# Kernel optimization log

Measured on AMD Instinct MI355X. Metric: run time of the kernel, lower is better.

The kernel has to match this reference:

```python
import jax, jax.numpy as jnp
import numpy as np

B, S, D = 4, 8192, 1024

def log_g(x):
    # log of g(x): log(x + 0.5) for x >= 0, log(sigmoid(x)) = -softplus(-x) otherwise
    return jnp.where(x >= 0, jnp.log(jax.nn.relu(x) + 0.5), -jax.nn.softplus(-x))

def setup_inputs() -> dict:
    key = jax.random.key(0)
    k1, k2 = jax.random.split(key)
    x = jax.random.normal(k1, (B, S, D), dtype=jnp.float32)
    # Linear(dim, 3*dim, bias=False); stored as [dim, 3*dim] so y = x @ W
    W = jax.random.normal(k2, (D, 3 * D), dtype=jnp.float32) * (1.0 / np.sqrt(D))
    return {"x": x, "W": W}

def reference(x, W):
    # x: [B, S, D], W: [D, 3D]
    hW = jnp.einsum('bsd,de->bse', x, W)  # [B, S, 3D]
    hidden, f_gate, i_gate = jnp.split(hW, 3, axis=-1)

    # log-space normalized gates:
    # diff = softplus(-f) - softplus(-i); log_f' = -softplus(diff); log_i' = -softplus(-diff)
    diff = jax.nn.softplus(-f_gate) - jax.nn.softplus(-i_gate)
    log_f = -jax.nn.softplus(diff)
    log_i = -jax.nn.softplus(-diff)
    log_values = log_i + log_g(hidden)

    # Heinsen associative scan in log space (float32 internally)
    a_star = jnp.cumsum(log_f.astype(jnp.float32), axis=1)
    log_h0_plus_b_star = jax.lax.cumlogsumexp(log_values.astype(jnp.float32) - a_star, axis=1)
    log_h = a_star + log_h0_plus_b_star
    out = jnp.exp(log_h).astype(x.dtype)  # [B, S, D]
    return out
```

## Files before the change

kernel.cpp:

```cpp
#include <hip/hip_runtime.h>
#include <hip/hip_bf16.h>
#include <cstdint>
#include <cstddef>


#define BB 4
#define SS 8192
#define DD 1024
#define MM 32768
#define KK 1024
#define NN 3072
#define CHUNKS 256
#define CLEN 32
#define NCH 4096
#define NT 16

typedef __bf16 bf16;
typedef __bf16 bf16x2 __attribute__((ext_vector_type(2)));
typedef __bf16 bf16x4 __attribute__((ext_vector_type(4)));
typedef __bf16 bf16x8 __attribute__((ext_vector_type(8)));
typedef float f32x4 __attribute__((ext_vector_type(4)));

__device__ __forceinline__ void gload16(const bf16* g, bf16* l) {
  __builtin_amdgcn_global_load_lds(
      (const __attribute__((address_space(1))) unsigned int*)(const void*)g,
      (__attribute__((address_space(3))) unsigned int*)(void*)l,
      16, 0, 0);
}

#if __has_builtin(__builtin_amdgcn_exp2f)
#define EXP2(x) __builtin_amdgcn_exp2f(x)
#else
#define EXP2(x) __expf((x) * 0.69314718056f)
#endif

__device__ __forceinline__ void gate2(float h, float f, float i,
                                      float& F, float& IG) {
  const float NL2E = -1.44269504089f;
  float P = EXP2(fminf(f * NL2E, 60.f));
  float Q = EXP2(fminf(i * NL2E, 60.f));
  float H = EXP2(fminf(h * NL2E, 60.f));
  float rZ = __builtin_amdgcn_rcpf(2.f + P + Q);
  float gh = (h >= 0.f) ? (h + 0.5f) : __builtin_amdgcn_rcpf(1.f + H);
  F = (1.f + Q) * rZ;
  IG = (1.f + P) * gh * rZ;
}

__device__ __forceinline__ float laddexp(float a, float b) {
  float m = fmaxf(a, b);
  return m + __logf(1.f + __expf(fminf(a, b) - m));
}
__device__ __forceinline__ void comb(float& A, float& V, float Ac, float Vc) {
  V = laddexp(V + Ac, Vc);
  A += Ac;
}

__global__ __launch_bounds__(256) void k_cvt_x(const float4* __restrict__ x,
                                               bf16x4* __restrict__ xb) {
  int i = blockIdx.x * 256 + threadIdx.x;
  float4 v = x[i];
  bf16x4 o;
  o[0] = (bf16)v.x; o[1] = (bf16)v.y; o[2] = (bf16)v.z; o[3] = (bf16)v.w;
  xb[i] = o;
}

__global__ __launch_bounds__(256) void k_cvt_wt(const float* __restrict__ W,
                                                bf16* __restrict__ Wt) {
  __shared__ float tile[32][33];
  int n0 = blockIdx.x * 32, k0 = blockIdx.y * 32;
  int tx = threadIdx.x, ty = threadIdx.y;
#pragma unroll
  for (int i = 0; i < 32; i += 8)
    tile[ty + i][tx] = W[(size_t)(k0 + ty + i) * NN + n0 + tx];
  __syncthreads();
#pragma unroll
  for (int i = 0; i < 32; i += 8)
    Wt[(size_t)(n0 + ty + i) * KK + k0 + tx] = (bf16)tile[tx][ty + i];
}

__global__ __launch_bounds__(512, 2) void k_gemm(const bf16* __restrict__ A,
                                                 const bf16* __restrict__ Bt,
                                                 bf16* __restrict__ C) {
  __shared__ __align__(16) bf16 sm[65536];
  const int tid = threadIdx.x;
  const int lane = tid & 63;
  const int w = tid >> 6;
  const int wm = w >> 2;
  const int wn = w & 3;
  const int c16 = lane & 15;
  const int l4 = lane >> 4;

  int bid = blockIdx.x;
  int swz = (bid & 7) * 192 + (bid >> 3);
  int mT = swz / 12;
  int nT = swz - mT * 12;
  const int mBase = mT * 256, nBase = nT * 256;

  const int sr = tid >> 3;
  const int scol = ((tid & 7) ^ (sr & 7)) * 8;
  const bf16* gA = A + (size_t)(mBase + sr) * KK + scol;
  const bf16* gB = Bt + (size_t)(nBase + sr) * KK + scol;
  const int ld = tid * 8;

  const int sw8 = c16 & 7;
  const int sx0 = (l4 ^ sw8) * 8;
  const int sx1 = ((l4 + 4) ^ sw8) * 8;
  const int aRow = (wm * 64 + c16) * 64;
  const int bRow = (wn * 32 + c16) * 64;

  f32x4 acc[2][2][4][2];
#pragma unroll
  for (int a = 0; a < 2; ++a)
#pragma unroll
    for (int b2 = 0; b2 < 2; ++b2)
#pragma unroll
      for (int m = 0; m < 4; ++m)
#pragma unroll
        for (int n = 0; n < 2; ++n)
          acc[a][b2][m][n] = (f32x4){0.f, 0.f, 0.f, 0.f};

#define STGA(h, L, bo, ko) \
  gload16(gA + (h) * 131072 + (L) * 65536 + (ko), \
          sm + (bo) + (h) * 8192 + (L) * 4096 + ld)
#define STGB(h, L, bo, ko) \
  gload16(gB + (h) * 131072 + (L) * 65536 + (ko), \
          sm + (bo) + 16384 + (h) * 8192 + (L) * 4096 + ld)
#define LDA(qm, AF)                                                     \
  _Pragma("unroll") for (int mi = 0; mi < 4; ++mi) {                    \
    const bf16* p_ = sm + buf + (qm) * 8192 + aRow + mi * 1024;         \
    AF[mi][0] = *(const bf16x8*)(p_ + sx0);                             \
    AF[mi][1] = *(const bf16x8*)(p_ + sx1);                             \
  }
#define LDB(qn, BF)                                                     \
  _Pragma("unroll") for (int ni = 0; ni < 2; ++ni) {                    \
    const bf16* p_ = sm + buf + 16384 + (qn) * 8192 + bRow + ni * 1024; \
    BF[ni][0] = *(const bf16x8*)(p_ + sx0);                             \
    BF[ni][1] = *(const bf16x8*)(p_ + sx1);                             \
  }
#define MFMAQ(qm, qn, AF, BF)                                             \
  __builtin_amdgcn_s_setprio(1);                                          \
  _Pragma("unroll") for (int mi = 0; mi < 4; ++mi)                        \
  _Pragma("unroll") for (int ni = 0; ni < 2; ++ni) {                      \
    acc[qm][qn][mi][ni] = __builtin_amdgcn_mfma_f32_16x16x32_bf16(        \
        AF[mi][0], BF[ni][0], acc[qm][qn][mi][ni], 0, 0, 0);              \
    acc[qm][qn][mi][ni] = __builtin_amdgcn_mfma_f32_16x16x32_bf16(        \
        AF[mi][1], BF[ni][1], acc[qm][qn][mi][ni], 0, 0, 0);              \
  }                                                                       \
  __builtin_amdgcn_s_setprio(0);
#define BAR asm volatile("s_barrier" ::: "memory")
#define VMC(n) asm volatile("s_waitcnt vmcnt(" #n ")" ::: "memory")

  STGA(0, 0, 0, 0); STGA(0, 1, 0, 0); STGB(0, 0, 0, 0); STGB(0, 1, 0, 0);
  STGA(1, 0, 0, 0); STGA(1, 1, 0, 0); STGB(1, 0, 0, 0); STGB(1, 1, 0, 0);
  VMC(4);
  BAR;

  bf16x8 afr[4][2], bfr0[2][2], bfr1[2][2];

  for (int t = 0; t < NT - 1; ++t) {
    const int buf = (t & 1) << 15;
    const int nb = buf ^ 32768;
    const int ko = (t + 1) * 64;
    LDA(0, afr); LDB(0, bfr0);
    STGA(0, 0, nb, ko); STGA(0, 1, nb, ko);
    STGB(0, 0, nb, ko); STGB(0, 1, nb, ko);
    VMC(4);
    BAR;
    MFMAQ(0, 0, afr, bfr0);
    LDB(1, bfr1);
    STGA(1, 0, nb, ko); STGA(1, 1, nb, ko);
    MFMAQ(0, 1, afr, bfr1);
    LDA(1, afr);
    STGB(1, 0, nb, ko); STGB(1, 1, nb, ko);
    MFMAQ(1, 1, afr, bfr1);
    VMC(4);
    BAR;
    MFMAQ(1, 0, afr, bfr0);
  }
  {
    const int buf = 32768;
    LDA(0, afr); LDB(0, bfr0);
    VMC(0);
    BAR;
    MFMAQ(0, 0, afr, bfr0);
    LDB(1, bfr1);
    MFMAQ(0, 1, afr, bfr1);
    LDA(1, afr);
    MFMAQ(1, 1, afr, bfr1);
    MFMAQ(1, 0, afr, bfr0);
  }

  __syncthreads();
  const int rq = l4 * 4;
#pragma unroll
  for (int qm = 0; qm < 2; ++qm)
#pragma unroll
    for (int qn = 0; qn < 2; ++qn)
#pragma unroll
      for (int mi = 0; mi < 4; ++mi)
#pragma unroll
        for (int ni = 0; ni < 2; ++ni)
#pragma unroll
          for (int r = 0; r < 4; ++r) {
            int row = qm * 128 + wm * 64 + mi * 16 + rq + r;
            int col = (qn * 128 + wn * 32 + ni * 16 + c16) ^ ((row & 7) << 3);
            sm[row * 256 + col] = (bf16)acc[qm][qn][mi][ni][r];
          }
  __syncthreads();
#pragma unroll
  for (int p = 0; p < 16; ++p) {
    int row = p * 16 + (tid >> 5);
    int colL = (tid & 31) * 8;
    int col = colL ^ ((row & 7) << 3);
    bf16x8 v = *(const bf16x8*)(sm + row * 256 + col);
    *(bf16x8*)(C + (size_t)(mBase + row) * NN + nBase + colL) = v;
  }
#undef STGA
#undef STGB
#undef LDA
#undef LDB
#undef MFMAQ
#undef BAR
#undef VMC
}

__global__ __launch_bounds__(256) void k_scan1(const bf16* __restrict__ hW,
                                               float2* __restrict__ agg) {
  const int d0 = threadIdx.x * 4;
  const int b = blockIdx.y, c = blockIdx.z;
  const bf16* p = hW + (size_t)(b * SS + c * CLEN) * NN + d0;
  float Fp[4] = {1.f, 1.f, 1.f, 1.f};
  float v[4] = {0.f, 0.f, 0.f, 0.f};
  bf16x4 hA = *(const bf16x4*)(p);
  bf16x4 fA = *(const bf16x4*)(p + DD);
  bf16x4 iA = *(const bf16x4*)(p + 2 * DD);
  const bf16* p1 = p + NN;
  bf16x4 hB = *(const bf16x4*)(p1);
  bf16x4 fB = *(const bf16x4*)(p1 + DD);
  bf16x4 iB = *(const bf16x4*)(p1 + 2 * DD);
  p += 2 * NN;
#pragma unroll 2
  for (int j = 0; j < CLEN - 2; ++j) {
    bf16x4 hn = *(const bf16x4*)(p);
    bf16x4 fn = *(const bf16x4*)(p + DD);
    bf16x4 in2 = *(const bf16x4*)(p + 2 * DD);
    p += NN;
#pragma unroll
    for (int e = 0; e < 4; ++e) {
      float F, IG;
      gate2((float)hA[e], (float)fA[e], (float)iA[e], F, IG);
      v[e] = fmaf(v[e], F, IG);
      Fp[e] *= F;
    }
    hA = hB; fA = fB; iA = iB;
    hB = hn; fB = fn; iB = in2;
  }
#pragma unroll
  for (int e = 0; e < 4; ++e) {
    float F, IG;
    gate2((float)hA[e], (float)fA[e], (float)iA[e], F, IG);
    v[e] = fmaf(v[e], F, IG);
    Fp[e] *= F;
  }
#pragma unroll
  for (int e = 0; e < 4; ++e) {
    float F, IG;
    gate2((float)hB[e], (float)fB[e], (float)iB[e], F, IG);
    v[e] = fmaf(v[e], F, IG);
    Fp[e] *= F;
  }
  const size_t ch = (size_t)b * DD + d0;
#pragma unroll
  for (int e = 0; e < 4; ++e)
    agg[(ch + e) * CHUNKS + c] =
        make_float2(__logf(fmaxf(Fp[e], 1e-37f)), __logf(fmaxf(v[e], 1e-37f)));
}

__global__ __launch_bounds__(256) void k_scan2(const float2* __restrict__ agg,
                                               float2* __restrict__ pre) {
  const int ch = blockIdx.x * 4 + (threadIdx.x >> 6);
  const int lane = threadIdx.x & 63;
  const float4* src = (const float4*)(agg + (size_t)ch * CHUNKS);
  float4 v0 = src[lane * 2];
  float4 v1 = src[lane * 2 + 1];
  float A = v0.x, V = v0.y;
  comb(A, V, v0.z, v0.w);
  comb(A, V, v1.x, v1.y);
  comb(A, V, v1.z, v1.w);
#pragma unroll
  for (int off = 1; off < 64; off <<= 1) {
    float Ao = __shfl_up(A, off);
    float Vo = __shfl_up(V, off);
    if (lane >= off) {
      V = laddexp(Vo + A, V);
      A = Ao + A;
    }
  }
  float exA = __shfl_up(A, 1);
  float exV = __shfl_up(V, 1);
  if (lane == 0) { exA = 0.f; exV = -1e30f; }
  float4 o0, o1;
  o0.x = exA; o0.y = exV;
  comb(exA, exV, v0.x, v0.y);
  o0.z = exA; o0.w = exV;
  comb(exA, exV, v0.z, v0.w);
  o1.x = exA; o1.y = exV;
  comb(exA, exV, v1.x, v1.y);
  o1.z = exA; o1.w = exV;
  float4* dst = (float4*)(pre + (size_t)ch * CHUNKS);
  dst[lane * 2] = o0;
  dst[lane * 2 + 1] = o1;
}

__global__ __launch_bounds__(256) void k_scan3(const bf16* __restrict__ hW,
                                               const float2* __restrict__ pre,
                                               float* __restrict__ out) {
  const int d0 = threadIdx.x * 4;
  const int b = blockIdx.y, c = blockIdx.z;
  const bf16* p = hW + (size_t)(b * SS + c * CLEN) * NN + d0;
  float* o = out + (size_t)(b * SS + c * CLEN) * DD + d0;
  const size_t ch = (size_t)b * DD + d0;
  float v[4];
#pragma unroll
  for (int e = 0; e < 4; ++e)
    v[e] = __expf(pre[(ch + e) * CHUNKS + c].y);
  bf16x4 hA = *(const bf16x4*)(p);
  bf16x4 fA = *(const bf16x4*)(p + DD);
  bf16x4 iA = *(const bf16x4*)(p + 2 * DD);
  const bf16* p1 = p + NN;
  bf16x4 hB = *(const bf16x4*)(p1);
  bf16x4 fB = *(const bf16x4*)(p1 + DD);
  bf16x4 iB = *(const bf16x4*)(p1 + 2 * DD);
  p += 2 * NN;
#pragma unroll 2
  for (int j = 0; j < CLEN - 2; ++j) {
    bf16x4 hn = *(const bf16x4*)(p);
    bf16x4 fn = *(const bf16x4*)(p + DD);
    bf16x4 in2 = *(const bf16x4*)(p + 2 * DD);
    p += NN;
    float4 ov;
#pragma unroll
    for (int e = 0; e < 4; ++e) {
      float F, IG;
      gate2((float)hA[e], (float)fA[e], (float)iA[e], F, IG);
      v[e] = fmaf(v[e], F, IG);
    }
    ov.x = v[0]; ov.y = v[1]; ov.z = v[2]; ov.w = v[3];
    *(float4*)o = ov;
    o += DD;
    hA = hB; fA = fB; iA = iB;
    hB = hn; fB = fn; iB = in2;
  }
  {
    float4 ov;
#pragma unroll
    for (int e = 0; e < 4; ++e) {
      float F, IG;
      gate2((float)hA[e], (float)fA[e], (float)iA[e], F, IG);
      v[e] = fmaf(v[e], F, IG);
    }
    ov.x = v[0]; ov.y = v[1]; ov.z = v[2]; ov.w = v[3];
    *(float4*)o = ov;
    o += DD;
  }
  {
    float4 ov;
#pragma unroll
    for (int e = 0; e < 4; ++e) {
      float F, IG;
      gate2((float)hB[e], (float)fB[e], (float)iB[e], F, IG);
      v[e] = fmaf(v[e], F, IG);
    }
    ov.x = v[0]; ov.y = v[1]; ov.z = v[2]; ov.w = v[3];
    *(float4*)o = ov;
  }
}

extern "C" void kernel_launch(void* const* d_in, const int* in_sizes, int n_in,
                              void* d_out, int out_size, void* d_ws,
                              size_t ws_size, hipStream_t stream) {
  const float* x = (const float*)d_in[0];
  const float* W = (const float*)d_in[1];
  float* out = (float*)d_out;
  char* ws = (char*)d_ws;

  const size_t wtB = (size_t)NN * KK * 2;
  const size_t xbB = (size_t)MM * KK * 2;
  const size_t aggB = (size_t)CHUNKS * NCH * sizeof(float2);
  bf16* Wt = (bf16*)ws;
  bf16* xb = (bf16*)(ws + wtB);
  bf16* hW = (bf16*)(ws + wtB + xbB);
  float2* agg = (float2*)(ws + wtB);
  float2* pre = (float2*)(ws + wtB + aggB);

  k_cvt_wt<<<dim3(NN / 32, KK / 32), dim3(32, 8), 0, stream>>>(W, Wt);
  k_cvt_x<<<dim3(MM * KK / 4 / 256), dim3(256), 0, stream>>>((const float4*)x,
                                                             (bf16x4*)xb);
  k_gemm<<<dim3((NN / 256) * (MM / 256)), 512, 0, stream>>>(xb, Wt, hW);
  k_scan1<<<dim3(1, BB, CHUNKS), 256, 0, stream>>>(hW, agg);
  k_scan2<<<dim3(NCH / 4), 256, 0, stream>>>(agg, pre);
  k_scan3<<<dim3(1, BB, CHUNKS), 256, 0, stream>>>(hW, pre, out);
}
```

Baseline: 528.2 us.

## Fuse three scan kernels into one cooperative kernel with grid syncs

Replaces the three scan launches with a single cooperative kernel that runs chunk aggregation, the cross-chunk prefix, and the final pass, separated by grid-wide barriers. It also transposes the agg/pre layout to chunk-major so phase 1 and phase 3 accesses are contiguous per block. The aim is to remove launch gaps between kernels and possibly let the hW chunk stay in cache between phases. It requires all 1024 blocks to be co-resident (launch_bounds 256,4) and falls back to the separate kernels if the cooperative launch fails. Grid syncs and the strided atomic loads in phase 2 add their own cost.

```diff
diff --git a/kernel.cpp b/kernel.cpp
--- a/kernel.cpp
+++ b/kernel.cpp
@@ -1,8 +1,11 @@
 #include <hip/hip_runtime.h>
 #include <hip/hip_bf16.h>
+#include <hip/hip_cooperative_groups.h>
 #include <cstdint>
 #include <cstddef>
 
+
+namespace cg = cooperative_groups;
 
 #define BB 4
 #define SS 8192
@@ -33,6 +36,14 @@
 #else
 #define EXP2(x) __expf((x) * 0.69314718056f)
 #endif
+
+__device__ __forceinline__ float2 aload(const float2* p) {
+  unsigned long long u = __hip_atomic_load(
+      (const unsigned long long*)p, __ATOMIC_RELAXED, __HIP_MEMORY_SCOPE_AGENT);
+  union { unsigned long long u; float2 f; } c;
+  c.u = u;
+  return c.f;
+}
 
 __device__ __forceinline__ void gate2(float h, float f, float i,
                                       float& F, float& IG) {
@@ -224,10 +235,11 @@
 #undef VMC
 }
 
-__global__ __launch_bounds__(256) void k_scan1(const bf16* __restrict__ hW,
-                                               float2* __restrict__ agg) {
-  const int d0 = threadIdx.x * 4;
-  const int b = blockIdx.y, c = blockIdx.z;
+
+__device__ __forceinline__ void scan_phase1(const bf16* __restrict__ hW,
+                                            float2* __restrict__ agg,
+                                            int b, int c, int tid) {
+  const int d0 = tid * 4;
   const bf16* p = hW + (size_t)(b * SS + c * CLEN) * NN + d0;
   float Fp[4] = {1.f, 1.f, 1.f, 1.f};
   float v[4] = {0.f, 0.f, 0.f, 0.f};
@@ -269,24 +281,23 @@
     v[e] = fmaf(v[e], F, IG);
     Fp[e] *= F;
   }
-  const size_t ch = (size_t)b * DD + d0;
+  float2* wout = agg + (size_t)c * NCH + b * DD + d0;
 #pragma unroll
   for (int e = 0; e < 4; ++e)
-    agg[(ch + e) * CHUNKS + c] =
+    wout[e] =
         make_float2(__logf(fmaxf(Fp[e], 1e-37f)), __logf(fmaxf(v[e], 1e-37f)));
 }
 
-__global__ __launch_bounds__(256) void k_scan2(const float2* __restrict__ agg,
-                                               float2* __restrict__ pre) {
-  const int ch = blockIdx.x * 4 + (threadIdx.x >> 6);
-  const int lane = threadIdx.x & 63;
-  const float4* src = (const float4*)(agg + (size_t)ch * CHUNKS);
-  float4 v0 = src[lane * 2];
-  float4 v1 = src[lane * 2 + 1];
-  float A = v0.x, V = v0.y;
-  comb(A, V, v0.z, v0.w);
-  comb(A, V, v1.x, v1.y);
-  comb(A, V, v1.z, v1.w);
+__device__ __forceinline__ void scan_phase2(const float2* __restrict__ agg,
+                                            float2* __restrict__ pre,
+                                            int widx, int lane) {
+  float2 vv[4];
+#pragma unroll
+  for (int q = 0; q < 4; ++q)
+    vv[q] = aload(agg + (size_t)(lane * 4 + q) * NCH + widx);
+  float A = vv[0].x, V = vv[0].y;
+#pragma unroll
+  for (int q = 1; q < 4; ++q) comb(A, V, vv[q].x, vv[q].y);
 #pragma unroll
   for (int off = 1; off < 64; off <<= 1) {
     float Ao = __shfl_up(A, off);
@@ -299,31 +310,25 @@
   float exA = __shfl_up(A, 1);
   float exV = __shfl_up(V, 1);
   if (lane == 0) { exA = 0.f; exV = -1e30f; }
-  float4 o0, o1;
-  o0.x = exA; o0.y = exV;
-  comb(exA, exV, v0.x, v0.y);
-  o0.z = exA; o0.w = exV;
-  comb(exA, exV, v0.z, v0.w);
-  o1.x = exA; o1.y = exV;
-  comb(exA, exV, v1.x, v1.y);
-  o1.z = exA; o1.w = exV;
-  float4* dst = (float4*)(pre + (size_t)ch * CHUNKS);
-  dst[lane * 2] = o0;
-  dst[lane * 2 + 1] = o1;
-}
-
-__global__ __launch_bounds__(256) void k_scan3(const bf16* __restrict__ hW,
-                                               const float2* __restrict__ pre,
-                                               float* __restrict__ out) {
-  const int d0 = threadIdx.x * 4;
-  const int b = blockIdx.y, c = blockIdx.z;
+#pragma unroll
+  for (int q = 0; q < 4; ++q) {
+    pre[(size_t)(lane * 4 + q) * NCH + widx] = make_float2(exA, exV);
+    comb(exA, exV, vv[q].x, vv[q].y);
+  }
+}
+
+__device__ __forceinline__ void scan_phase3(const bf16* __restrict__ hW,
+                                            const float2* __restrict__ pre,
+                                            float* __restrict__ out,
+                                            int b, int c, int tid) {
+  const int d0 = tid * 4;
   const bf16* p = hW + (size_t)(b * SS + c * CLEN) * NN + d0;
   float* o = out + (size_t)(b * SS + c * CLEN) * DD + d0;
-  const size_t ch = (size_t)b * DD + d0;
+  const float2* pr = pre + (size_t)c * NCH + b * DD + d0;
   float v[4];
 #pragma unroll
   for (int e = 0; e < 4; ++e)
-    v[e] = __expf(pre[(ch + e) * CHUNKS + c].y);
+    v[e] = __expf(aload(pr + e).y);
   bf16x4 hA = *(const bf16x4*)(p);
   bf16x4 fA = *(const bf16x4*)(p + DD);
   bf16x4 iA = *(const bf16x4*)(p + 2 * DD);
@@ -376,6 +381,35 @@
   }
 }
 
+__global__ __launch_bounds__(256, 4) void k_scan_fused(
+    const bf16* __restrict__ hW, float2* __restrict__ agg,
+    float2* __restrict__ pre, float* __restrict__ out) {
+  const int tid = threadIdx.x;
+  const int b = blockIdx.y, c = blockIdx.z;
+  cg::grid_group g = cg::this_grid();
+  scan_phase1(hW, agg, b, c, tid);
+  __threadfence();
+  g.sync();
+  scan_phase2(agg, pre, (c * BB + b) * 4 + (tid >> 6), tid & 63);
+  __threadfence();
+  g.sync();
+  scan_phase3(hW, pre, out, b, c, tid);
+}
+
+__global__ __launch_bounds__(256) void k_scan1(const bf16* __restrict__ hW,
+                                               float2* __restrict__ agg) {
+  scan_phase1(hW, agg, blockIdx.y, blockIdx.z, threadIdx.x);
+}
+__global__ __launch_bounds__(256) void k_scan2(const float2* __restrict__ agg,
+                                               float2* __restrict__ pre) {
+  scan_phase2(agg, pre, blockIdx.x * 4 + (threadIdx.x >> 6), threadIdx.x & 63);
+}
+__global__ __launch_bounds__(256) void k_scan3(const bf16* __restrict__ hW,
+                                               const float2* __restrict__ pre,
+                                               float* __restrict__ out) {
+  scan_phase3(hW, pre, out, blockIdx.y, blockIdx.z, threadIdx.x);
+}
+
 extern "C" void kernel_launch(void* const* d_in, const int* in_sizes, int n_in,
                               void* d_out, int out_size, void* d_ws,
                               size_t ws_size, hipStream_t stream) {
@@ -397,7 +431,16 @@
   k_cvt_x<<<dim3(MM * KK / 4 / 256), dim3(256), 0, stream>>>((const float4*)x,
                                                              (bf16x4*)xb);
   k_gemm<<<dim3((NN / 256) * (MM / 256)), 512, 0, stream>>>(xb, Wt, hW);
-  k_scan1<<<dim3(1, BB, CHUNKS), 256, 0, stream>>>(hW, agg);
-  k_scan2<<<dim3(NCH / 4), 256, 0, stream>>>(agg, pre);
-  k_scan3<<<dim3(1, BB, CHUNKS), 256, 0, stream>>>(hW, pre, out);
-}
+
+  {
+    void* args[] = {(void*)&hW, (void*)&agg, (void*)&pre, (void*)&out};
+    hipError_t e = hipLaunchCooperativeKernel(
+        (void*)k_scan_fused, dim3(1, BB, CHUNKS), dim3(256, 1, 1), args, 0,
+        stream);
+    if (e != hipSuccess) {
+      k_scan1<<<dim3(1, BB, CHUNKS), 256, 0, stream>>>(hW, agg);
+      k_scan2<<<dim3(NCH / 4), 256, 0, stream>>>(agg, pre);
+      k_scan3<<<dim3(1, BB, CHUNKS), 256, 0, stream>>>(hW, pre, out);
+    }
+  }
+}
```

Result: slower. 987.8 us (+87.0%).
